# Optimization experiments

Hardware: AMD Instinct MI355X
Metric: run time of the kernel (lower is better)

## Reference

```python
import jax, jax.numpy as jnp
import numpy as np

B, T, C = 4, 2048, 2048
H, D = 16, 128  # n_heads, head_dim


def _rope_freqs(seq_len, head_dim, base=10000.0):
    half = head_dim // 2
    inv = 1.0 / (base ** (np.arange(half, dtype=np.float32) / half))
    t = np.arange(seq_len, dtype=np.float32)
    ang = np.outer(t, inv)  # (T, D/2)
    return jnp.asarray(np.stack([np.cos(ang), np.sin(ang)], axis=-1))  # (T, D/2, 2)


def setup_inputs() -> dict:
    key = jax.random.key(0)
    k1, k2, k3 = jax.random.split(key, 3)
    x = jax.random.normal(k1, (B, T, C), dtype=jnp.float32)
    freqs = _rope_freqs(T, D)
    # additive causal mask
    mask = jnp.where(jnp.tril(jnp.ones((T, T), dtype=bool)), 0.0, -1e9).astype(jnp.float32)
    w_qkv = jax.random.normal(k2, (3 * C, C), dtype=jnp.float32) * (1.0 / np.sqrt(C))
    w_out = jax.random.normal(k3, (C, C), dtype=jnp.float32) * (1.0 / np.sqrt(C))
    return {"x": x, "freqs": freqs, "mask": mask, "w_qkv": w_qkv, "w_out": w_out}


def apply_rope(x, freqs):
    # x: (B,H,T,D), freqs: (T,D/2,2)
    xr = x.reshape(*x.shape[:-1], -1, 2)
    cos, sin = freqs[..., 0], freqs[..., 1]
    x0, x1 = xr[..., 0], xr[..., 1]
    rot = jnp.stack([x0 * cos - x1 * sin, x0 * sin + x1 * cos], axis=-1)
    return rot.reshape(x.shape)


def reference(x, freqs, mask, w_qkv, w_out):
    b, t, c = x.shape
    qkv = jnp.einsum('btc,fc->btf', x, w_qkv).reshape(b, t, 3, H, D)
    q, k, v = jnp.moveaxis(qkv, 2, 0)          # each (b,t,H,D)
    q = jnp.transpose(q, (0, 2, 1, 3))          # (b,H,t,D)
    k = jnp.transpose(k, (0, 2, 1, 3))
    v = jnp.transpose(v, (0, 2, 1, 3))
    q = apply_rope(q, freqs[:t])
    k = apply_rope(k, freqs[:t])
    scale = 1.0 / np.sqrt(D).astype(np.float32)
    attn = jnp.einsum('bhqd,bhkd->bhqk', q, k) * scale + mask[:t, :t]
    attn = jax.nn.softmax(attn, axis=-1)
    out = jnp.einsum('bhqk,bhkd->bhqd', attn, v)
    out = jnp.transpose(out, (0, 2, 1, 3)).reshape(b, t, c)
    return jnp.einsum('btc,fc->btf', out, w_out)
```

## Files before the change

### kernel.cpp

```cpp
#include <hip/hip_runtime.h>

typedef unsigned short u16;
typedef unsigned int   u32;

using sx8   = __attribute__((ext_vector_type(8))) short;
using f32x4 = __attribute__((ext_vector_type(4))) float;
using u16x8 = __attribute__((ext_vector_type(8))) unsigned short;

#define BB 4
#define TT 2048
#define CC 2048
#define HH 16
#define DD 128
#define FF 6144
#define MM 8192

static __device__ __forceinline__ u16 f2bf(float f) {
    u32 u = __builtin_bit_cast(u32, f);
    u32 lsb = (u >> 16) & 1u;
    u += 0x7fffu + lsb;
    return (u16)(u >> 16);
}
static __device__ __forceinline__ float bf2f(u16 b) {
    return __builtin_bit_cast(float, (u32)b << 16);
}
static __device__ __forceinline__ f32x4 mfma16(sx8 a, sx8 b, f32x4 c) {
    return __builtin_amdgcn_mfma_f32_16x16x32_bf16(a, b, c, 0, 0, 0);
}
static __device__ __forceinline__ u32 pkbf(float a, float b) {
    return (u32)f2bf(a) | ((u32)f2bf(b) << 16);
}

__global__ __launch_bounds__(256) void k_cvt(const float* __restrict__ src,
                                             u16* __restrict__ dst, int n8) {
    int i = blockIdx.x * 256 + threadIdx.x;
    if (i >= n8) return;
    const float4* s = (const float4*)src;
    float4 a = s[2 * (size_t)i], b = s[2 * (size_t)i + 1];
    u16x8 r;
    r[0] = f2bf(a.x); r[1] = f2bf(a.y); r[2] = f2bf(a.z); r[3] = f2bf(a.w);
    r[4] = f2bf(b.x); r[5] = f2bf(b.y); r[6] = f2bf(b.z); r[7] = f2bf(b.w);
    *(u16x8*)(dst + 8 * (size_t)i) = r;
}

template <int MODE>
__global__ __launch_bounds__(256, 2) void k_gemm(const u16* __restrict__ A,
                                                 const u16* __restrict__ Bt,
                                                 float* __restrict__ Cf,
                                                 const float* __restrict__ freqs,
                                                 u16* __restrict__ Qo,
                                                 u16* __restrict__ Ko,
                                                 u16* __restrict__ Vt,
                                                 int M, int N, int K) {
    __shared__ __align__(16) u16 sA[128 * 32];
    __shared__ __align__(16) u16 sB[128 * 32];
    __shared__ __align__(16) u16 vT[4][64][17];
    const int n0 = blockIdx.x * 128, m0 = blockIdx.y * 128;
    const int tid = threadIdx.x, w = tid >> 6, l = tid & 63;
    const int wm = w >> 1, wn = w & 1;
    const int lr = l & 15, lg = l >> 4;
    f32x4 acc[4][4] = {};

    const int idx0 = w * 128 + l;
    const int idx1 = idx0 + 64;
    const int ra0 = idx0 >> 2, ca0 = (idx0 & 3) * 8;
    const int ra1 = idx1 >> 2, ca1 = (idx1 & 3) * 8;
    const u16* Ar0 = A + (size_t)(m0 + ra0) * K + ca0;
    const u16* Ar1 = A + (size_t)(m0 + ra1) * K + ca1;
    const u16* Br0 = Bt + (size_t)(n0 + ra0) * K + ca0;
    const u16* Br1 = Bt + (size_t)(n0 + ra1) * K + ca1;
    u16* sAd0 = sA + (w * 2 + 0) * 512;
    u16* sAd1 = sA + (w * 2 + 1) * 512;
    u16* sBd0 = sB + (w * 2 + 0) * 512;
    u16* sBd1 = sB + (w * 2 + 1) * 512;

    for (int k0 = 0; k0 < K; k0 += 32) {
        __builtin_amdgcn_global_load_lds(
            (const __attribute__((address_space(1))) void*)(Ar0 + k0),
            (__attribute__((address_space(3))) void*)sAd0, 16, 0, 0);
        __builtin_amdgcn_global_load_lds(
            (const __attribute__((address_space(1))) void*)(Ar1 + k0),
            (__attribute__((address_space(3))) void*)sAd1, 16, 0, 0);
        __builtin_amdgcn_global_load_lds(
            (const __attribute__((address_space(1))) void*)(Br0 + k0),
            (__attribute__((address_space(3))) void*)sBd0, 16, 0, 0);
        __builtin_amdgcn_global_load_lds(
            (const __attribute__((address_space(1))) void*)(Br1 + k0),
            (__attribute__((address_space(3))) void*)sBd1, 16, 0, 0);
        __syncthreads();
        sx8 af[4], bfr[4];
#pragma unroll
        for (int i = 0; i < 4; i++)
            af[i] = *(const sx8*)(sA + (wm * 64 + i * 16 + lr) * 32 + lg * 8);
#pragma unroll
        for (int j = 0; j < 4; j++)
            bfr[j] = *(const sx8*)(sB + (wn * 64 + j * 16 + lr) * 32 + lg * 8);
#pragma unroll
        for (int i = 0; i < 4; i++)
#pragma unroll
            for (int j = 0; j < 4; j++)
                acc[i][j] = mfma16(af[i], bfr[j], acc[i][j]);
        __syncthreads();
    }

    if (MODE == 1) {
#pragma unroll
        for (int i = 0; i < 4; i++) {
            const int mr = m0 + wm * 64 + i * 16 + lg * 4;
#pragma unroll
            for (int j = 0; j < 4; j++) {
                const int nc = n0 + wn * 64 + j * 16 + lr;
#pragma unroll
                for (int rg = 0; rg < 4; rg++)
                    Cf[(size_t)(mr + rg) * N + nc] = acc[i][j][rg];
            }
        }
    } else {
        const int b = m0 >> 11;
        const int t0blk = m0 & 2047;
        const int kind = n0 >> 11;
        const int h = (n0 & 2047) >> 7;
        const size_t bh = (size_t)(b * HH + h);
        if (kind < 2) {
            u16* dst = (kind == 0 ? Qo : Ko) + bh * (size_t)(TT * DD);
            const float qs = (kind == 0) ? 0.08838834764831845f : 1.0f;
#pragma unroll
            for (int i = 0; i < 4; i++) {
#pragma unroll
                for (int j = 0; j < 4; j++) {
                    const int d = wn * 64 + j * 16 + lr;
                    const int dp2 = (d >> 1) * 2;
#pragma unroll
                    for (int rg = 0; rg < 4; rg++) {
                        const int t = t0blk + wm * 64 + i * 16 + lg * 4 + rg;
                        float v = acc[i][j][rg];
                        float p = __shfl_xor(v, 1);
                        float2 cs = *(const float2*)(freqs + (size_t)t * DD + dp2);
                        float r = (lr & 1) ? (p * cs.y + v * cs.x)
                                           : (v * cs.x - p * cs.y);
                        dst[(size_t)t * DD + d] = f2bf(r * qs);
                    }
                }
            }
        } else {
            u16* dstV = Vt + bh * (size_t)(DD * TT);
            const int t0w = t0blk + wm * 64;
            const int dl = l >> 2, seg = l & 3;
#pragma unroll
            for (int j = 0; j < 4; ++j) {
#pragma unroll
                for (int i = 0; i < 4; ++i)
#pragma unroll
                    for (int rg = 0; rg < 4; ++rg)
                        vT[w][i * 16 + lg * 4 + rg][lr] = f2bf(acc[i][j][rg]);
                asm volatile("s_waitcnt lgkmcnt(0)" ::: "memory");
                __builtin_amdgcn_sched_barrier(0);
                u16x8 t2[2];
#pragma unroll
                for (int jj = 0; jj < 16; ++jj)
                    t2[jj >> 3][jj & 7] = vT[w][seg * 16 + jj][dl];
                const int dg = wn * 64 + j * 16 + dl;
                u16* orow = dstV + (size_t)dg * TT + t0w + seg * 16;
                *(u16x8*)orow = t2[0];
                *((u16x8*)orow + 1) = t2[1];
                asm volatile("s_waitcnt lgkmcnt(0)" ::: "memory");
                __builtin_amdgcn_sched_barrier(0);
            }
        }
    }
}

#define KV 64
#define PST 68

__global__ __launch_bounds__(256, 2) void k_attn(const u16* __restrict__ Q,
                                                 const u16* __restrict__ K,
                                                 const u16* __restrict__ Vt,
                                                 u16* __restrict__ AO) {
    const int fid = blockIdx.x + 8 * blockIdx.y + 128 * blockIdx.z;
    const int xg = fid >> 6;
    const int hb = fid & 63;
    const int h = hb & 15, b = hb >> 4;

    const int tid = threadIdx.x, w = tid >> 6, l = tid & 63;
    const int lr = l & 15, lg = l >> 4;
    const size_t bh = (size_t)(b * HH + h);
    const u16* Qh = Q + bh * TT * DD;
    const u16* Kh = K + bh * TT * DD;
    const u16* Vh = Vt + bh * DD * TT;

    __shared__ __align__(16) u16 sK[2][KV * DD];
    __shared__ __align__(16) u16 sP[4][32 * PST];
    u16* myP = sP[w];

    const int strow = tid >> 4;
    const int sc16  = tid & 15;

    for (int rep = 0; rep < 2; ++rep) {
        const int g = rep ? (15 - xg) : xg;
        const int q0w = g * 128 + w * 32;
        const int nt = 2 * g + 2;

        sx8 qf[2][4];
#pragma unroll
        for (int i = 0; i < 2; i++)
#pragma unroll
            for (int kk = 0; kk < 4; kk++)
                qf[i][kk] = *(const sx8*)(Qh + (size_t)(q0w + i * 16 + lr) * DD + kk * 32 + lg * 8);

        f32x4 o[2][8] = {};
        float mrow[2] = {-1e30f, -1e30f};
        float lrow[2] = {0.0f, 0.0f};

#pragma unroll
        for (int i = 0; i < 4; ++i) {
            const int row = i * 16 + strow;
            const int scol = (sc16 ^ (row & 7)) * 8;
            __builtin_amdgcn_global_load_lds(
                (const __attribute__((address_space(1))) void*)(Kh + (size_t)row * DD + scol),
                (__attribute__((address_space(3))) void*)(&sK[0][i * 2048 + w * 512]),
                16, 0, 0);
        }
        __syncthreads();

        int cur = 0;
        for (int t = 0; t < nt; ++t) {
            const int k0 = t * KV;
            if (t + 1 < nt) {
                const int kn = k0 + KV;
#pragma unroll
                for (int i = 0; i < 4; ++i) {
                    const int row = i * 16 + strow;
                    const int scol = (sc16 ^ (row & 7)) * 8;
                    __builtin_amdgcn_global_load_lds(
                        (const __attribute__((address_space(1))) void*)(Kh + (size_t)(kn + row) * DD + scol),
                        (__attribute__((address_space(3))) void*)(&sK[cur ^ 1][i * 2048 + w * 512]),
                        16, 0, 0);
                }
            }
            if (k0 <= q0w) {
                f32x4 st[2][4] = {};
#pragma unroll
                for (int j = 0; j < 4; ++j) {
                    const int row = j * 16 + lr;
                    const int rx = row & 7;
                    sx8 kf[4];
#pragma unroll
                    for (int kk = 0; kk < 4; ++kk) {
                        const int c16 = (kk * 4 + lg) ^ rx;
                        kf[kk] = *(const sx8*)(&sK[cur][row * DD + c16 * 8]);
                    }
#pragma unroll
                    for (int kk = 0; kk < 4; ++kk) {
                        st[0][j] = mfma16(kf[kk], qf[0][kk], st[0][j]);
                        st[1][j] = mfma16(kf[kk], qf[1][kk], st[1][j]);
                    }
                }
                sx8 vf0[8];
#pragma unroll
                for (int n = 0; n < 8; ++n)
                    vf0[n] = *(const sx8*)(Vh + (size_t)(n * 16 + lr) * TT + k0 + lg * 8);

                const bool need_mask = (k0 + 63 > q0w);
                const int klocal = lg * 4;
#pragma unroll
                for (int i = 0; i < 2; ++i) {
                    if (need_mask) {
                        const int cl = q0w + i * 16 + lr - k0;
#pragma unroll
                        for (int j = 0; j < 4; ++j)
#pragma unroll
                            for (int rg = 0; rg < 4; ++rg)
                                if (j * 16 + klocal + rg > cl) st[i][j][rg] = -1e30f;
                    }
                    f32x4 m4;
#pragma unroll
                    for (int rg = 0; rg < 4; ++rg)
                        m4[rg] = fmaxf(fmaxf(st[i][0][rg], st[i][1][rg]),
                                       fmaxf(st[i][2][rg], st[i][3][rg]));
                    float pm = fmaxf(fmaxf(m4[0], m4[1]), fmaxf(m4[2], m4[3]));
                    pm = fmaxf(pm, __shfl_xor(pm, 16));
                    pm = fmaxf(pm, __shfl_xor(pm, 32));
                    const float mold = mrow[i];
                    const bool resc = pm > mold + 8.0f;
                    const float mnew = resc ? pm : mold;
                    mrow[i] = mnew;
                    float rs = 0.0f;
#pragma unroll
                    for (int j = 0; j < 4; ++j) {
                        float p0 = __expf(st[i][j][0] - mnew);
                        float p1 = __expf(st[i][j][1] - mnew);
                        float p2 = __expf(st[i][j][2] - mnew);
                        float p3 = __expf(st[i][j][3] - mnew);
                        rs += (p0 + p1) + (p2 + p3);
                        *(uint2*)(myP + (i * 16 + lr) * PST + j * 16 + klocal) =
                            make_uint2(pkbf(p0, p1), pkbf(p2, p3));
                    }
                    rs += __shfl_xor(rs, 16);
                    rs += __shfl_xor(rs, 32);
                    const float sf = resc ? __expf(mold - mnew) : 1.0f;
                    lrow[i] = lrow[i] * sf + rs;
                    if (__any(resc)) {
                        f32x4 sfo;
#pragma unroll
                        for (int rg = 0; rg < 4; ++rg)
                            sfo[rg] = __shfl(sf, 4 * lg + rg);
#pragma unroll
                        for (int n = 0; n < 8; ++n) o[i][n] *= sfo;
                    }
                }
                asm volatile("s_waitcnt lgkmcnt(0)" ::: "memory");
                __builtin_amdgcn_sched_barrier(0);

                sx8 pa0[2], pa1[2];
                pa0[0] = *(const sx8*)(myP + (size_t)lr * PST + lg * 8);
                pa0[1] = *(const sx8*)(myP + (size_t)(16 + lr) * PST + lg * 8);
                pa1[0] = *(const sx8*)(myP + (size_t)lr * PST + 32 + lg * 8);
                pa1[1] = *(const sx8*)(myP + (size_t)(16 + lr) * PST + 32 + lg * 8);
#pragma unroll
                for (int n = 0; n < 8; ++n) {
                    o[0][n] = mfma16(pa0[0], vf0[n], o[0][n]);
                    o[1][n] = mfma16(pa0[1], vf0[n], o[1][n]);
                }
#pragma unroll
                for (int n = 0; n < 8; ++n) {
                    sx8 vf1 = *(const sx8*)(Vh + (size_t)(n * 16 + lr) * TT + k0 + 32 + lg * 8);
                    o[0][n] = mfma16(pa1[0], vf1, o[0][n]);
                    o[1][n] = mfma16(pa1[1], vf1, o[1][n]);
                }
            }
            __syncthreads();
            cur ^= 1;
        }

#pragma unroll
        for (int i = 0; i < 2; ++i) {
            f32x4 linv;
#pragma unroll
            for (int rg = 0; rg < 4; ++rg)
                linv[rg] = __shfl(lrow[i], 4 * lg + rg);
#pragma unroll
            for (int rg = 0; rg < 4; ++rg) {
                const float inv = 1.0f / linv[rg];
                const int tq = q0w + i * 16 + lg * 4 + rg;
                u16* orow = AO + ((size_t)(b * TT) + tq) * CC + h * DD + lr;
#pragma unroll
                for (int n = 0; n < 8; ++n)
                    orow[n * 16] = f2bf(o[i][n][rg] * inv);
            }
        }
    }
}

extern "C" void kernel_launch(void* const* d_in, const int* in_sizes, int n_in,
                              void* d_out, int out_size, void* d_ws, size_t ws_size,
                              hipStream_t stream) {
    const float* x     = (const float*)d_in[0];
    const float* freqs = (const float*)d_in[1];
    const float* w_qkv = (const float*)d_in[3];
    const float* w_out = (const float*)d_in[4];
    float* out = (float*)d_out;

    u16* ws   = (u16*)d_ws;
    u16* xb   = ws;
    u16* wqb  = xb   + (size_t)MM * CC;
    u16* wob  = wqb  + (size_t)FF * CC;
    u16* AO   = wob  + (size_t)CC * CC;
    u16* Qr   = AO   + (size_t)MM * CC;
    u16* Kr   = Qr   + (size_t)MM * CC;
    u16* Vt   = Kr   + (size_t)MM * CC;

    k_cvt<<<MM * CC / 2048, 256, 0, stream>>>(x, xb, MM * CC / 8);
    k_cvt<<<FF * CC / 2048, 256, 0, stream>>>(w_qkv, wqb, FF * CC / 8);
    k_cvt<<<CC * CC / 2048, 256, 0, stream>>>(w_out, wob, CC * CC / 8);

    k_gemm<2><<<dim3(FF / 128, MM / 128), 256, 0, stream>>>(
        xb, wqb, nullptr, freqs, Qr, Kr, Vt, MM, FF, CC);
    k_attn<<<dim3(8, HH, BB), 256, 0, stream>>>(Qr, Kr, Vt, AO);
    k_gemm<1><<<dim3(CC / 128, MM / 128), 256, 0, stream>>>(
        AO, wob, out, nullptr, nullptr, nullptr, nullptr, MM, CC, CC);
}
```

Measured before the change: 520.4 us.

## Switch GEMMs to 32x32x16 MFMA and merge three fp32-to-bf16 conversions

The GEMM kernel now uses 32x32x16 bf16 MFMA tiles (2x2 per wave) instead of 16x16x32 tiles (4x4 per wave), so each wave issues fewer matrix instructions and fewer LDS fragment reads per k-step. The epilogues (plain store, RoPE for Q/K, and V transpose through LDS) are rewritten for the 32x32 accumulator layout, and the V staging buffer grows to 33 columns. The three conversion kernels are merged into one launch over the contiguous workspace to save launch overhead. The larger accumulator layout changes the global store pattern in the epilogues and may affect coalescing.

```diff
diff --git a/kernel.cpp b/kernel.cpp
--- a/kernel.cpp
+++ b/kernel.cpp
@@ -3,9 +3,10 @@
 typedef unsigned short u16;
 typedef unsigned int   u32;
 
-using sx8   = __attribute__((ext_vector_type(8))) short;
-using f32x4 = __attribute__((ext_vector_type(4))) float;
-using u16x8 = __attribute__((ext_vector_type(8))) unsigned short;
+using sx8    = __attribute__((ext_vector_type(8))) short;
+using f32x4  = __attribute__((ext_vector_type(4))) float;
+using f32x16 = __attribute__((ext_vector_type(16))) float;
+using u16x8  = __attribute__((ext_vector_type(8))) unsigned short;
 
 #define BB 4
 #define TT 2048
@@ -27,20 +28,32 @@
 static __device__ __forceinline__ f32x4 mfma16(sx8 a, sx8 b, f32x4 c) {
     return __builtin_amdgcn_mfma_f32_16x16x32_bf16(a, b, c, 0, 0, 0);
 }
+static __device__ __forceinline__ f32x16 mfma32(sx8 a, sx8 b, f32x16 c) {
+    return __builtin_amdgcn_mfma_f32_32x32x16_bf16(a, b, c, 0, 0, 0);
+}
 static __device__ __forceinline__ u32 pkbf(float a, float b) {
     return (u32)f2bf(a) | ((u32)f2bf(b) << 16);
 }
 
-__global__ __launch_bounds__(256) void k_cvt(const float* __restrict__ src,
-                                             u16* __restrict__ dst, int n8) {
-    int i = blockIdx.x * 256 + threadIdx.x;
-    if (i >= n8) return;
-    const float4* s = (const float4*)src;
-    float4 a = s[2 * (size_t)i], b = s[2 * (size_t)i + 1];
+__global__ __launch_bounds__(256) void k_cvt3(const float* __restrict__ x,
+                                              const float* __restrict__ wq,
+                                              const float* __restrict__ wo,
+                                              u16* __restrict__ dst) {
+    const size_t n0 = (size_t)MM * CC / 8, n1 = n0 + (size_t)FF * CC / 8;
+    const size_t n2 = n1 + (size_t)CC * CC / 8;
+    size_t i = (size_t)blockIdx.x * 256 + threadIdx.x;
+    if (i >= n2) return;
+    const float* s;
+    size_t off;
+    if (i < n0)      { s = x;  off = i; }
+    else if (i < n1) { s = wq; off = i - n0; }
+    else             { s = wo; off = i - n1; }
+    const float4* sp = (const float4*)s;
+    float4 a = sp[2 * off], b = sp[2 * off + 1];
     u16x8 r;
     r[0] = f2bf(a.x); r[1] = f2bf(a.y); r[2] = f2bf(a.z); r[3] = f2bf(a.w);
     r[4] = f2bf(b.x); r[5] = f2bf(b.y); r[6] = f2bf(b.z); r[7] = f2bf(b.w);
-    *(u16x8*)(dst + 8 * (size_t)i) = r;
+    *(u16x8*)(dst + 8 * i) = r;
 }
 
 template <int MODE>
@@ -54,12 +67,12 @@
                                                  int M, int N, int K) {
     __shared__ __align__(16) u16 sA[128 * 32];
     __shared__ __align__(16) u16 sB[128 * 32];
-    __shared__ __align__(16) u16 vT[4][64][17];
+    __shared__ __align__(16) u16 vT[4][64][33];
     const int n0 = blockIdx.x * 128, m0 = blockIdx.y * 128;
     const int tid = threadIdx.x, w = tid >> 6, l = tid & 63;
     const int wm = w >> 1, wn = w & 1;
-    const int lr = l & 15, lg = l >> 4;
-    f32x4 acc[4][4] = {};
+    const int l31 = l & 31, hi = l >> 5;
+    f32x16 acc[2][2] = {};
 
     const int idx0 = w * 128 + l;
     const int idx1 = idx0 + 64;
@@ -88,33 +101,36 @@
             (const __attribute__((address_space(1))) void*)(Br1 + k0),
             (__attribute__((address_space(3))) void*)sBd1, 16, 0, 0);
         __syncthreads();
-        sx8 af[4], bfr[4];
-#pragma unroll
-        for (int i = 0; i < 4; i++)
-            af[i] = *(const sx8*)(sA + (wm * 64 + i * 16 + lr) * 32 + lg * 8);
-#pragma unroll
-        for (int j = 0; j < 4; j++)
-            bfr[j] = *(const sx8*)(sB + (wn * 64 + j * 16 + lr) * 32 + lg * 8);
-#pragma unroll
-        for (int i = 0; i < 4; i++)
-#pragma unroll
-            for (int j = 0; j < 4; j++)
-                acc[i][j] = mfma16(af[i], bfr[j], acc[i][j]);
+        sx8 af[2][2], bfr[2][2];
+#pragma unroll
+        for (int ti = 0; ti < 2; ++ti)
+#pragma unroll
+            for (int ks = 0; ks < 2; ++ks) {
+                af[ti][ks]  = *(const sx8*)(sA + (wm * 64 + ti * 32 + l31) * 32 + ks * 16 + hi * 8);
+                bfr[ti][ks] = *(const sx8*)(sB + (wn * 64 + ti * 32 + l31) * 32 + ks * 16 + hi * 8);
+            }
+#pragma unroll
+        for (int ks = 0; ks < 2; ++ks)
+#pragma unroll
+            for (int ti = 0; ti < 2; ++ti)
+#pragma unroll
+                for (int tj = 0; tj < 2; ++tj)
+                    acc[ti][tj] = mfma32(af[ti][ks], bfr[tj][ks], acc[ti][tj]);
         __syncthreads();
     }
 
     if (MODE == 1) {
 #pragma unroll
-        for (int i = 0; i < 4; i++) {
-            const int mr = m0 + wm * 64 + i * 16 + lg * 4;
-#pragma unroll
-            for (int j = 0; j < 4; j++) {
-                const int nc = n0 + wn * 64 + j * 16 + lr;
-#pragma unroll
-                for (int rg = 0; rg < 4; rg++)
-                    Cf[(size_t)(mr + rg) * N + nc] = acc[i][j][rg];
-            }
-        }
+        for (int ti = 0; ti < 2; ++ti)
+#pragma unroll
+            for (int tj = 0; tj < 2; ++tj) {
+                const int nc = n0 + wn * 64 + tj * 32 + l31;
+#pragma unroll
+                for (int r = 0; r < 16; ++r) {
+                    const int mr = m0 + wm * 64 + ti * 32 + (r & 3) + 8 * (r >> 2) + 4 * hi;
+                    Cf[(size_t)mr * N + nc] = acc[ti][tj][r];
+                }
+            }
     } else {
         const int b = m0 >> 11;
         const int t0blk = m0 & 2047;
@@ -125,44 +141,46 @@
             u16* dst = (kind == 0 ? Qo : Ko) + bh * (size_t)(TT * DD);
             const float qs = (kind == 0) ? 0.08838834764831845f : 1.0f;
 #pragma unroll
-            for (int i = 0; i < 4; i++) {
-#pragma unroll
-                for (int j = 0; j < 4; j++) {
-                    const int d = wn * 64 + j * 16 + lr;
+            for (int ti = 0; ti < 2; ++ti)
+#pragma unroll
+                for (int tj = 0; tj < 2; ++tj) {
+                    const int d = wn * 64 + tj * 32 + l31;
                     const int dp2 = (d >> 1) * 2;
 #pragma unroll
-                    for (int rg = 0; rg < 4; rg++) {
-                        const int t = t0blk + wm * 64 + i * 16 + lg * 4 + rg;
-                        float v = acc[i][j][rg];
+                    for (int r = 0; r < 16; ++r) {
+                        const int t = t0blk + wm * 64 + ti * 32 + (r & 3) + 8 * (r >> 2) + 4 * hi;
+                        float v = acc[ti][tj][r];
                         float p = __shfl_xor(v, 1);
                         float2 cs = *(const float2*)(freqs + (size_t)t * DD + dp2);
-                        float r = (lr & 1) ? (p * cs.y + v * cs.x)
+                        float rr = (l & 1) ? (p * cs.y + v * cs.x)
                                            : (v * cs.x - p * cs.y);
-                        dst[(size_t)t * DD + d] = f2bf(r * qs);
-                    }
-                }
-            }
+                        dst[(size_t)t * DD + d] = f2bf(rr * qs);
+                    }
+                }
         } else {
             u16* dstV = Vt + bh * (size_t)(DD * TT);
             const int t0w = t0blk + wm * 64;
-            const int dl = l >> 2, seg = l & 3;
-#pragma unroll
-            for (int j = 0; j < 4; ++j) {
-#pragma unroll
-                for (int i = 0; i < 4; ++i)
-#pragma unroll
-                    for (int rg = 0; rg < 4; ++rg)
-                        vT[w][i * 16 + lg * 4 + rg][lr] = f2bf(acc[i][j][rg]);
+            const int dl = l >> 1, seg = l & 1;
+#pragma unroll
+            for (int tj = 0; tj < 2; ++tj) {
+#pragma unroll
+                for (int ti = 0; ti < 2; ++ti)
+#pragma unroll
+                    for (int r = 0; r < 16; ++r)
+                        vT[w][ti * 32 + (r & 3) + 8 * (r >> 2) + 4 * hi][l31] =
+                            f2bf(acc[ti][tj][r]);
                 asm volatile("s_waitcnt lgkmcnt(0)" ::: "memory");
                 __builtin_amdgcn_sched_barrier(0);
-                u16x8 t2[2];
-#pragma unroll
-                for (int jj = 0; jj < 16; ++jj)
-                    t2[jj >> 3][jj & 7] = vT[w][seg * 16 + jj][dl];
-                const int dg = wn * 64 + j * 16 + dl;
-                u16* orow = dstV + (size_t)dg * TT + t0w + seg * 16;
-                *(u16x8*)orow = t2[0];
-                *((u16x8*)orow + 1) = t2[1];
+                const int dg = wn * 64 + tj * 32 + dl;
+                u16* orow = dstV + (size_t)dg * TT + t0w + seg * 32;
+#pragma unroll
+                for (int half = 0; half < 4; ++half) {
+                    u16x8 t2;
+#pragma unroll
+                    for (int jj = 0; jj < 8; ++jj)
+                        t2[jj] = vT[w][seg * 32 + half * 8 + jj][dl];
+                    *(u16x8*)(orow + half * 8) = t2;
+                }
                 asm volatile("s_waitcnt lgkmcnt(0)" ::: "memory");
                 __builtin_amdgcn_sched_barrier(0);
             }
@@ -370,9 +388,8 @@
     u16* Kr   = Qr   + (size_t)MM * CC;
     u16* Vt   = Kr   + (size_t)MM * CC;
 
-    k_cvt<<<MM * CC / 2048, 256, 0, stream>>>(x, xb, MM * CC / 8);
-    k_cvt<<<FF * CC / 2048, 256, 0, stream>>>(w_qkv, wqb, FF * CC / 8);
-    k_cvt<<<CC * CC / 2048, 256, 0, stream>>>(w_out, wob, CC * CC / 8);
+    const int ncv = (MM * CC + FF * CC + CC * CC) / 8;
+    k_cvt3<<<(ncv + 255) / 256, 256, 0, stream>>>(x, w_qkv, w_out, xb);
 
     k_gemm<2><<<dim3(FF / 128, MM / 128), 256, 0, stream>>>(
         xb, wqb, nullptr, freqs, Qr, Kr, Vt, MM, FF, CC);
```

Measured after the change: 551.9 us. +6.1%, slower.
